# Performance work log

Measured on AMD Instinct MI355X. Metric: run time of the kernel, lower is better.

The kernel has to match this reference:

```python
import jax, jax.numpy as jnp
import numpy as np
from jax import lax

K = 3
PAD = 1


def setup_inputs() -> dict:
    key = jax.random.key(0)
    k1, k2, k3 = jax.random.split(key, 3)
    B, Cin, Cout, H, W = 4, 64, 64, 128, 128
    x = jax.random.normal(k1, (B, Cin, H, W), dtype=jnp.float32)
    # offset-predicting conv params (2*K*K output channels); small init keeps offsets modest
    offset_w = jax.random.normal(k2, (2 * K * K, Cin, K, K), dtype=jnp.float32) * 0.05
    offset_b = jnp.zeros((2 * K * K,), dtype=jnp.float32)
    # deformable conv weight/bias (module uses randn weight, zero bias)
    weight = jax.random.normal(k3, (Cout, Cin, K, K), dtype=jnp.float32) * 0.05
    bias = jnp.zeros((Cout,), dtype=jnp.float32)
    return {"x": x, "offset_w": offset_w, "offset_b": offset_b, "weight": weight, "bias": bias}


def _conv2d(x, w, b):
    y = lax.conv_general_dilated(x, w, window_strides=(1, 1),
                                 padding=((PAD, PAD), (PAD, PAD)),
                                 dimension_numbers=("NCHW", "OIHW", "NCHW"))
    return y + b[None, :, None, None]


def _bilinear_gather(x, py, px):
    # x: [B,C,H,W]; py,px: [B,KK,HO,WO] sample coords -> [B,C,KK,HO,WO], zeros outside
    B, C, H, W = x.shape
    y0 = jnp.floor(py)
    x0 = jnp.floor(px)
    ly = py - y0
    lx = px - x0
    y0i = y0.astype(jnp.int32)
    x0i = x0.astype(jnp.int32)
    xf = x.reshape(B, C, H * W)

    def corner(yi, xi, w):
        mask = ((yi >= 0) & (yi < H) & (xi >= 0) & (xi < W)).astype(x.dtype)
        lin = jnp.clip(yi, 0, H - 1) * W + jnp.clip(xi, 0, W - 1)  # [B,KK,HO,WO]
        g = jax.vmap(lambda xb, ib: xb[:, ib])(xf, lin)            # [B,C,KK,HO,WO]
        return g * (w * mask)[:, None]

    return (corner(y0i, x0i, (1 - ly) * (1 - lx))
            + corner(y0i, x0i + 1, (1 - ly) * lx)
            + corner(y0i + 1, x0i, ly * (1 - lx))
            + corner(y0i + 1, x0i + 1, ly * lx))


def reference(x, offset_w, offset_b, weight, bias):
    B, Cin, H, W = x.shape
    Cout = weight.shape[0]
    KK = K * K
    offset = _conv2d(x, offset_w, offset_b)            # [B, 2*KK, H, W]
    off = offset.reshape(B, KK, 2, H, W)               # torchvision layout: (dy, dx) per tap
    dy, dx = off[:, :, 0], off[:, :, 1]                # [B,KK,H,W]
    ki = (jnp.arange(KK) // K).astype(x.dtype)
    kj = (jnp.arange(KK) % K).astype(x.dtype)
    hs = jnp.arange(H, dtype=x.dtype)
    ws = jnp.arange(W, dtype=x.dtype)
    base_y = ki[:, None, None] + hs[None, :, None] - PAD   # [KK,H,1]
    base_x = kj[:, None, None] + ws[None, None, :] - PAD   # [KK,1,W]
    py = dy + base_y[None]                             # [B,KK,H,W]
    px = dx + base_x[None]
    sampled = _bilinear_gather(x, py, px)              # [B,Cin,KK,H,W]
    out = jnp.einsum("bckhw,ock->bohw", sampled, weight.reshape(Cout, Cin, KK))
    return out + bias[None, :, None, None]
```

## Files before the change

kernel.cpp:

```cpp
#include <hip/hip_runtime.h>

typedef _Float16 f16x8 __attribute__((ext_vector_type(8)));
typedef float f32x4 __attribute__((ext_vector_type(4)));

__device__ __forceinline__ f16x8 splat8(float v) {
  _Float16 h = (_Float16)v;
  return f16x8{h, h, h, h, h, h, h, h};
}

__device__ __forceinline__ int swzh(int i) { return i ^ (((i >> 6) & 7) << 3); }

__global__ __launch_bounds__(256) void k_xtprep(const float* __restrict__ x,
                                                const float* __restrict__ wt,
                                                const float* __restrict__ ow,
                                                _Float16* __restrict__ xt,
                                                _Float16* __restrict__ wb,
                                                _Float16* __restrict__ owb) {
  __shared__ float tile[64 * 65];
  int blk = blockIdx.x;
  int t = threadIdx.x;
  if (blk < 1024) {
    int b = blk >> 8;
    int y = (blk >> 1) & 127;
    int w0 = (blk & 1) * 64;
    const float* xp = x + ((size_t)(b * 64) * 128 + y) * 128 + w0;
#pragma unroll
    for (int it = 0; it < 4; ++it) {
      int idx = it * 256 + t;
      int c = idx >> 4, q = idx & 15;
      float4 v = *(const float4*)(xp + (size_t)c * 16384 + q * 4);
      float* tp = &tile[c * 65 + q * 4];
      tp[0] = v.x; tp[1] = v.y; tp[2] = v.z; tp[3] = v.w;
    }
    __syncthreads();
#pragma unroll
    for (int it = 0; it < 2; ++it) {
      int idx = it * 256 + t;
      int w = idx >> 3, c8 = idx & 7;
      f16x8 o;
#pragma unroll
      for (int j = 0; j < 8; ++j) o[j] = (_Float16)tile[(c8 * 8 + j) * 65 + w];
      *(f16x8*)&xt[(((size_t)b * 128 + y) * 128 + w0 + w) * 64 + c8 * 8] = o;
    }
  } else {
    int i = (blk - 1024) * 256 + t;
    if (i < 36864) {
      int k = i >> 12, rem = i & 4095, o = rem >> 6, c = rem & 63;
      wb[i] = (_Float16)wt[(o * 64 + c) * 9 + k];
    } else if (i < 36864 + 18432) {
      int j = i - 36864;
      int k = j >> 11, rem = j & 2047, o = rem >> 6, c = rem & 63;
      float v = (o < 18) ? ow[(o * 64 + c) * 9 + k] : 0.0f;
      owb[j] = (_Float16)v;
    }
  }
}

__global__ __launch_bounds__(512, 2) void k_fused(
    const _Float16* __restrict__ xt, const _Float16* __restrict__ wb,
    const _Float16* __restrict__ owb, const float* __restrict__ ob,
    const float* __restrict__ bias, float* __restrict__ out) {
  __shared__ char lds[75776];
  _Float16* Wp3 = (_Float16*)lds;
  _Float16* S = (_Float16*)(lds + 49152);
  _Float16* Xs = (_Float16*)lds;
  _Float16* owbL = (_Float16*)(lds + 26112);
  float* offL = (float*)(lds + 65536);

  int t = threadIdx.x;
  int lb = (blockIdx.x & 7) * 64 + (blockIdx.x >> 3);
  int w0 = (lb & 3) * 32;
  int h0 = ((lb >> 2) & 31) * 4;
  int b = lb >> 7;

  int lane = t & 63, wid = t >> 6;
  int lr = lane & 15, quad = lane >> 4;
  const _Float16* xb = xt + (size_t)b * 128 * 128 * 64;

#pragma unroll
  for (int it = 0; it < 4; ++it) {
    int idx8 = it * 512 + t;
    if (idx8 < 1632) {
      int c8 = idx8 & 7;
      int jr = idx8 >> 3;
      int col = jr % 34;
      int xr = jr / 34;
      int gy = h0 - 1 + xr;
      int gx = w0 - 1 + col;
      f16x8 v = {};
      if (((unsigned)gy < 128u) & ((unsigned)gx < 128u))
        v = *(const f16x8*)(xb + ((size_t)gy * 128 + gx) * 64 + c8 * 8);
      *(f16x8*)&Xs[swzh(jr * 64 + c8 * 8)] = v;
    }
  }
#pragma unroll
  for (int it = 0; it < 2; ++it) {
    int idx8 = it * 512 + t;
    if (idx8 < 768) {
      int kb = idx8 >> 8, rem = idx8 & 255;
      int o = rem >> 3, c8 = rem & 7;
      *(f16x8*)&owbL[swzh(kb * 2048 + o * 64 + c8 * 8)] =
          ((const f16x8*)(owb + kb * 2048))[rem];
    }
  }

  {
    int oh = (wid >> 2) * 16;
    int ar = wid & 3;
    f32x4 accA[2];
    accA[0] = f32x4{0.f, 0.f, 0.f, 0.f};
    accA[1] = f32x4{0.f, 0.f, 0.f, 0.f};
#pragma unroll
    for (int bt = 0; bt < 3; ++bt) {
      __syncthreads();
#pragma unroll
      for (int kb = 0; kb < 3; ++kb) {
        int ai = (bt & 1) * 6144 + kb * 2048 + (oh + lr) * 64 + quad * 8;
        f16x8 afr0 = *(const f16x8*)&owbL[swzh(ai)];
        f16x8 afr1 = *(const f16x8*)&owbL[swzh(ai + 32)];
#pragma unroll
        for (int ni = 0; ni < 2; ++ni) {
          int j = ni * 16 + lr + kb;
          int bi = ((ar + bt) * 34 + j) * 64 + quad * 8;
          f16x8 b0 = *(const f16x8*)&Xs[swzh(bi)];
          f16x8 b1 = *(const f16x8*)&Xs[swzh(bi + 32)];
          accA[ni] = __builtin_amdgcn_mfma_f32_16x16x32_f16(afr0, b0, accA[ni], 0, 0, 0);
          accA[ni] = __builtin_amdgcn_mfma_f32_16x16x32_f16(afr1, b1, accA[ni], 0, 0, 0);
        }
      }
      if (bt < 2) {
#pragma unroll
        for (int it = 0; it < 2; ++it) {
          int idx8 = it * 512 + t;
          if (idx8 < 768) {
            int kb = idx8 >> 8, rem = idx8 & 255;
            int o = rem >> 3, c8 = rem & 7;
            *(f16x8*)&owbL[swzh(((bt + 1) & 1) * 6144 + kb * 2048 + o * 64 + c8 * 8)] =
                ((const f16x8*)(owb + ((bt + 1) * 3 + kb) * 2048))[rem];
          }
        }
      }
    }
    int qr = quad * 4;
#pragma unroll
    for (int ni = 0; ni < 2; ++ni) {
#pragma unroll
      for (int r = 0; r < 4; ++r) {
        int co = oh + qr + r;
        if (co < 18) {
          int px = ar * 32 + ni * 16 + lr;
          offL[px * 20 + co] = accA[ni][r] + ob[co];
        }
      }
    }
  }
  __syncthreads();

  int pixS = t >> 2, cg = t & 3;
  int rS = pixS >> 5;
  int wS = w0 + (pixS & 31);
  int woB = (wid >> 2) * 32, wpB = (wid & 3) * 32;

  f32x4 acc[2][2];
#pragma unroll
  for (int i = 0; i < 2; ++i)
#pragma unroll
    for (int j = 0; j < 2; ++j) acc[i][j] = f32x4{0.f, 0.f, 0.f, 0.f};

#pragma unroll
  for (int it = 0; it < 3; ++it) {
    int idx8 = it * 512 + t;
    int kb = idx8 >> 9, rem = idx8 & 511;
    int o = rem >> 3, c8 = rem & 7;
    *(f16x8*)&Wp3[swzh(kb * 4096 + o * 64 + c8 * 8)] =
        ((const f16x8*)(wb + kb * 4096))[rem];
  }

#pragma unroll
  for (int k = 0; k < 9; ++k) {
    if (k == 1 || k == 4) {
      int bt = k / 3 + 1;
#pragma unroll
      for (int it = 0; it < 3; ++it) {
        int idx8 = it * 512 + t;
        int kb = idx8 >> 9, rem = idx8 & 511;
        int o = rem >> 3, c8 = rem & 7;
        *(f16x8*)&Wp3[swzh((bt & 1) * 12288 + kb * 4096 + o * 64 + c8 * 8)] =
            ((const f16x8*)(wb + (bt * 3 + kb) * 4096))[rem];
      }
    }
    {
      int ki = k / 3, kj = k % 3;
      float dy = offL[pixS * 20 + 2 * k];
      float dx = offL[pixS * 20 + 2 * k + 1];
      float py = dy + (float)(h0 + rS + ki - 1);
      float pxf = dx + (float)(wS + kj - 1);
      float fy = floorf(py), fx = floorf(pxf);
      float ly = py - fy, lx = pxf - fx;
      int y0 = (int)fy, x0 = (int)fx;
      int y1 = y0 + 1, x1 = x0 + 1;
      bool vy0 = (unsigned)y0 < 128u, vy1 = (unsigned)y1 < 128u;
      bool vx0 = (unsigned)x0 < 128u, vx1 = (unsigned)x1 < 128u;
      float w00 = (vy0 && vx0) ? (1.f - ly) * (1.f - lx) : 0.f;
      float w01 = (vy0 && vx1) ? (1.f - ly) * lx : 0.f;
      float w10 = (vy1 && vx0) ? ly * (1.f - lx) : 0.f;
      float w11 = (vy1 && vx1) ? ly * lx : 0.f;
      int yc0 = min(max(y0, 0), 127), yc1 = min(max(y1, 0), 127);
      int xc0 = min(max(x0, 0), 127), xc1 = min(max(x1, 0), 127);
      const _Float16* p00 = xb + (yc0 * 128 + xc0) * 64 + cg * 16;
      int dxo = (xc1 - xc0) * 64, dyo = (yc1 - yc0) * 8192;
      f16x8 ga0 = *(const f16x8*)(p00);
      f16x8 ga1 = *(const f16x8*)(p00 + 8);
      f16x8 gb0 = *(const f16x8*)(p00 + dxo);
      f16x8 gb1 = *(const f16x8*)(p00 + dxo + 8);
      f16x8 gc0 = *(const f16x8*)(p00 + dyo);
      f16x8 gc1 = *(const f16x8*)(p00 + dyo + 8);
      f16x8 gd0 = *(const f16x8*)(p00 + dyo + dxo);
      f16x8 gd1 = *(const f16x8*)(p00 + dyo + dxo + 8);
      f16x8 W00 = splat8(w00), W01 = splat8(w01);
      f16x8 W10 = splat8(w10), W11 = splat8(w11);
      f16x8 s0 = W00 * ga0 + W01 * gb0 + W10 * gc0 + W11 * gd0;
      f16x8 s1 = W00 * ga1 + W01 * gb1 + W10 * gc1 + W11 * gd1;
      int si = pixS * 64 + cg * 16;
      *(f16x8*)&S[swzh(si)] = s0;
      *(f16x8*)&S[swzh(si + 8)] = s1;
    }
    __syncthreads();
    {
      int wo = ((k / 3) & 1) * 12288 + (k % 3) * 4096;
#pragma unroll
      for (int ks = 0; ks < 2; ++ks) {
        int c0 = ks * 32 + quad * 8;
        f16x8 bfr[2], afr[2];
#pragma unroll
        for (int ni = 0; ni < 2; ++ni)
          bfr[ni] = *(const f16x8*)&S[swzh((wpB + ni * 16 + lr) * 64 + c0)];
#pragma unroll
        for (int mi = 0; mi < 2; ++mi)
          afr[mi] = *(const f16x8*)&Wp3[swzh(wo + (woB + mi * 16 + lr) * 64 + c0)];
#pragma unroll
        for (int mi = 0; mi < 2; ++mi)
#pragma unroll
          for (int ni = 0; ni < 2; ++ni)
            acc[mi][ni] = __builtin_amdgcn_mfma_f32_16x16x32_f16(
                afr[mi], bfr[ni], acc[mi][ni], 0, 0, 0);
      }
    }
    if (k < 8) __syncthreads();
  }

  {
    int col = lane & 15;
    int qr = quad * 4;
#pragma unroll
    for (int mi = 0; mi < 2; ++mi) {
#pragma unroll
      for (int ni = 0; ni < 2; ++ni) {
#pragma unroll
        for (int r = 0; r < 4; ++r) {
          int o = woB + mi * 16 + qr + r;
          int px = wpB + ni * 16 + col;
          out[(((size_t)b * 64 + o) * 128 + h0 + (px >> 5)) * 128 + w0 + (px & 31)] =
              acc[mi][ni][r] + bias[o];
        }
      }
    }
  }
}

extern "C" void kernel_launch(void* const* d_in, const int* in_sizes, int n_in,
                              void* d_out, int out_size, void* d_ws,
                              size_t ws_size, hipStream_t stream) {
  const float* x = (const float*)d_in[0];
  const float* ow = (const float*)d_in[1];
  const float* ob = (const float*)d_in[2];
  const float* wt = (const float*)d_in[3];
  const float* bias = (const float*)d_in[4];
  float* out = (float*)d_out;

  char* ws = (char*)d_ws;
  _Float16* xt = (_Float16*)ws;
  _Float16* wb = (_Float16*)(ws + 8388608);
  _Float16* owb = (_Float16*)(ws + 8388608 + 73728);

  k_xtprep<<<1240, 256, 0, stream>>>(x, wt, ow, xt, wb, owb);
  k_fused<<<512, 512, 0, stream>>>(xt, wb, owb, ob, bias, out);
}
```

Measured before the change: 35.82 us.

## Warp-specialize deform conv: producer waves sample next tap while consumers run MFMA

Splits the 8 waves into 4 producer waves that stage one tap's weights and bilinear-sample the next tap into a double-buffered LDS tile, and 4 consumer waves that run MFMAs on the current tap covering all 64 output channels. The aim is to overlap gather latency with matrix math and to shrink LDS from three-tap weight staging to two single-tap buffers. In exchange, half the threads do sampling, so each producer handles twice the channels, and consumers carry a larger accumulator tile. The critical path may become whichever role is slower.

```diff
diff --git a/kernel.cpp b/kernel.cpp
--- a/kernel.cpp
+++ b/kernel.cpp
@@ -60,12 +60,12 @@
     const _Float16* __restrict__ xt, const _Float16* __restrict__ wb,
     const _Float16* __restrict__ owb, const float* __restrict__ ob,
     const float* __restrict__ bias, float* __restrict__ out) {
-  __shared__ char lds[75776];
-  _Float16* Wp3 = (_Float16*)lds;
-  _Float16* S = (_Float16*)(lds + 49152);
+  __shared__ char lds[60928];
+  _Float16* Wt2 = (_Float16*)lds;
+  _Float16* S2 = (_Float16*)(lds + 16384);
   _Float16* Xs = (_Float16*)lds;
   _Float16* owbL = (_Float16*)(lds + 26112);
-  float* offL = (float*)(lds + 65536);
+  float* offL = (float*)(lds + 50688);
 
   int t = threadIdx.x;
   int lb = (blockIdx.x & 7) * 64 + (blockIdx.x >> 3);
@@ -156,109 +156,120 @@
   }
   __syncthreads();
 
-  int pixS = t >> 2, cg = t & 3;
-  int rS = pixS >> 5;
-  int wS = w0 + (pixS & 31);
-  int woB = (wid >> 2) * 32, wpB = (wid & 3) * 32;
-
-  f32x4 acc[2][2];
-#pragma unroll
-  for (int i = 0; i < 2; ++i)
+  int st = t & 255;
+  int pxS = st & 127, chh = st >> 7;
+  int rS = pxS >> 5;
+  int wS = w0 + (pxS & 31);
+  int wpB = (wid & 3) * 32;
+
+  f32x4 acc[4][2];
+#pragma unroll
+  for (int i = 0; i < 4; ++i)
 #pragma unroll
     for (int j = 0; j < 2; ++j) acc[i][j] = f32x4{0.f, 0.f, 0.f, 0.f};
 
-#pragma unroll
-  for (int it = 0; it < 3; ++it) {
-    int idx8 = it * 512 + t;
-    int kb = idx8 >> 9, rem = idx8 & 511;
-    int o = rem >> 3, c8 = rem & 7;
-    *(f16x8*)&Wp3[swzh(kb * 4096 + o * 64 + c8 * 8)] =
-        ((const f16x8*)(wb + kb * 4096))[rem];
-  }
+#define STAGE_W_TAP(KK)                                                       \
+  {                                                                           \
+    const f16x8* wsrc = (const f16x8*)(wb + (KK) * 4096);                     \
+    _Pragma("unroll") for (int it = 0; it < 2; ++it) {                        \
+      int idx8 = it * 256 + st;                                               \
+      int o = idx8 >> 3, c8 = idx8 & 7;                                       \
+      *(f16x8*)&Wt2[((KK) & 1) * 4096 + swzh(o * 64 + c8 * 8)] = wsrc[idx8];  \
+    }                                                                         \
+  }
+
+#define SAMPLE_TAP(KK)                                                        \
+  {                                                                           \
+    int ki = (KK) / 3, kj = (KK) % 3;                                         \
+    float dy = offL[pxS * 20 + 2 * (KK)];                                     \
+    float dx = offL[pxS * 20 + 2 * (KK) + 1];                                 \
+    float py = dy + (float)(h0 + rS + ki - 1);                                \
+    float pxf = dx + (float)(wS + kj - 1);                                    \
+    float fy = floorf(py), fx = floorf(pxf);                                  \
+    float ly = py - fy, lx = pxf - fx;                                        \
+    int y0 = (int)fy, x0 = (int)fx;                                           \
+    int y1 = y0 + 1, x1 = x0 + 1;                                             \
+    bool vy0 = (unsigned)y0 < 128u, vy1 = (unsigned)y1 < 128u;                \
+    bool vx0 = (unsigned)x0 < 128u, vx1 = (unsigned)x1 < 128u;                \
+    float w00 = (vy0 && vx0) ? (1.f - ly) * (1.f - lx) : 0.f;                 \
+    float w01 = (vy0 && vx1) ? (1.f - ly) * lx : 0.f;                         \
+    float w10 = (vy1 && vx0) ? ly * (1.f - lx) : 0.f;                         \
+    float w11 = (vy1 && vx1) ? ly * lx : 0.f;                                 \
+    int yc0 = min(max(y0, 0), 127), yc1 = min(max(y1, 0), 127);               \
+    int xc0 = min(max(x0, 0), 127), xc1 = min(max(x1, 0), 127);               \
+    const _Float16* p00 = xb + (yc0 * 128 + xc0) * 64 + chh * 32;             \
+    int dxo = (xc1 - xc0) * 64, dyo = (yc1 - yc0) * 8192;                     \
+    f16x8 g0[4], g1[4], g2[4], g3[4];                                         \
+    _Pragma("unroll") for (int j = 0; j < 4; ++j) {                           \
+      g0[j] = *(const f16x8*)(p00 + j * 8);                                   \
+      g1[j] = *(const f16x8*)(p00 + dxo + j * 8);                             \
+      g2[j] = *(const f16x8*)(p00 + dyo + j * 8);                             \
+      g3[j] = *(const f16x8*)(p00 + dyo + dxo + j * 8);                       \
+    }                                                                         \
+    f16x8 W00 = splat8(w00), W01 = splat8(w01);                               \
+    f16x8 W10 = splat8(w10), W11 = splat8(w11);                               \
+    _Float16* Sd = (_Float16*)&S2[((KK) & 1) * 8192];                         \
+    _Pragma("unroll") for (int j = 0; j < 4; ++j) {                           \
+      f16x8 s = W00 * g0[j] + W01 * g1[j] + W10 * g2[j] + W11 * g3[j];        \
+      *(f16x8*)&Sd[swzh(pxS * 64 + chh * 32 + j * 8)] = s;                    \
+    }                                                                         \
+  }
+
+  if (wid >= 4) {
+    STAGE_W_TAP(0)
+    SAMPLE_TAP(0)
+  }
+  __syncthreads();
 
 #pragma unroll
   for (int k = 0; k < 9; ++k) {
-    if (k == 1 || k == 4) {
-      int bt = k / 3 + 1;
-#pragma unroll
-      for (int it = 0; it < 3; ++it) {
-        int idx8 = it * 512 + t;
-        int kb = idx8 >> 9, rem = idx8 & 511;
-        int o = rem >> 3, c8 = rem & 7;
-        *(f16x8*)&Wp3[swzh((bt & 1) * 12288 + kb * 4096 + o * 64 + c8 * 8)] =
-            ((const f16x8*)(wb + (bt * 3 + kb) * 4096))[rem];
-      }
-    }
-    {
-      int ki = k / 3, kj = k % 3;
-      float dy = offL[pixS * 20 + 2 * k];
-      float dx = offL[pixS * 20 + 2 * k + 1];
-      float py = dy + (float)(h0 + rS + ki - 1);
-      float pxf = dx + (float)(wS + kj - 1);
-      float fy = floorf(py), fx = floorf(pxf);
-      float ly = py - fy, lx = pxf - fx;
-      int y0 = (int)fy, x0 = (int)fx;
-      int y1 = y0 + 1, x1 = x0 + 1;
-      bool vy0 = (unsigned)y0 < 128u, vy1 = (unsigned)y1 < 128u;
-      bool vx0 = (unsigned)x0 < 128u, vx1 = (unsigned)x1 < 128u;
-      float w00 = (vy0 && vx0) ? (1.f - ly) * (1.f - lx) : 0.f;
-      float w01 = (vy0 && vx1) ? (1.f - ly) * lx : 0.f;
-      float w10 = (vy1 && vx0) ? ly * (1.f - lx) : 0.f;
-      float w11 = (vy1 && vx1) ? ly * lx : 0.f;
-      int yc0 = min(max(y0, 0), 127), yc1 = min(max(y1, 0), 127);
-      int xc0 = min(max(x0, 0), 127), xc1 = min(max(x1, 0), 127);
-      const _Float16* p00 = xb + (yc0 * 128 + xc0) * 64 + cg * 16;
-      int dxo = (xc1 - xc0) * 64, dyo = (yc1 - yc0) * 8192;
-      f16x8 ga0 = *(const f16x8*)(p00);
-      f16x8 ga1 = *(const f16x8*)(p00 + 8);
-      f16x8 gb0 = *(const f16x8*)(p00 + dxo);
-      f16x8 gb1 = *(const f16x8*)(p00 + dxo + 8);
-      f16x8 gc0 = *(const f16x8*)(p00 + dyo);
-      f16x8 gc1 = *(const f16x8*)(p00 + dyo + 8);
-      f16x8 gd0 = *(const f16x8*)(p00 + dyo + dxo);
-      f16x8 gd1 = *(const f16x8*)(p00 + dyo + dxo + 8);
-      f16x8 W00 = splat8(w00), W01 = splat8(w01);
-      f16x8 W10 = splat8(w10), W11 = splat8(w11);
-      f16x8 s0 = W00 * ga0 + W01 * gb0 + W10 * gc0 + W11 * gd0;
-      f16x8 s1 = W00 * ga1 + W01 * gb1 + W10 * gc1 + W11 * gd1;
-      int si = pixS * 64 + cg * 16;
-      *(f16x8*)&S[swzh(si)] = s0;
-      *(f16x8*)&S[swzh(si + 8)] = s1;
-    }
-    __syncthreads();
-    {
-      int wo = ((k / 3) & 1) * 12288 + (k % 3) * 4096;
+    if (wid < 4) {
+      const _Float16* Wc = &Wt2[(k & 1) * 4096];
+      const _Float16* Sc = &S2[(k & 1) * 8192];
 #pragma unroll
       for (int ks = 0; ks < 2; ++ks) {
         int c0 = ks * 32 + quad * 8;
-        f16x8 bfr[2], afr[2];
+        f16x8 bfr[2], afr[4];
 #pragma unroll
         for (int ni = 0; ni < 2; ++ni)
-          bfr[ni] = *(const f16x8*)&S[swzh((wpB + ni * 16 + lr) * 64 + c0)];
-#pragma unroll
-        for (int mi = 0; mi < 2; ++mi)
-          afr[mi] = *(const f16x8*)&Wp3[swzh(wo + (woB + mi * 16 + lr) * 64 + c0)];
-#pragma unroll
-        for (int mi = 0; mi < 2; ++mi)
+          bfr[ni] = *(const f16x8*)&Sc[swzh((wpB + ni * 16 + lr) * 64 + c0)];
+#pragma unroll
+        for (int mi = 0; mi < 4; ++mi)
+          afr[mi] = *(const f16x8*)&Wc[swzh((mi * 16 + lr) * 64 + c0)];
+#pragma unroll
+        for (int mi = 0; mi < 4; ++mi)
 #pragma unroll
           for (int ni = 0; ni < 2; ++ni)
             acc[mi][ni] = __builtin_amdgcn_mfma_f32_16x16x32_f16(
                 afr[mi], bfr[ni], acc[mi][ni], 0, 0, 0);
       }
-    }
-    if (k < 8) __syncthreads();
-  }
-
-  {
+    } else if (k < 8) {
+      switch (k + 1) {
+        case 1: STAGE_W_TAP(1) SAMPLE_TAP(1) break;
+        case 2: STAGE_W_TAP(2) SAMPLE_TAP(2) break;
+        case 3: STAGE_W_TAP(3) SAMPLE_TAP(3) break;
+        case 4: STAGE_W_TAP(4) SAMPLE_TAP(4) break;
+        case 5: STAGE_W_TAP(5) SAMPLE_TAP(5) break;
+        case 6: STAGE_W_TAP(6) SAMPLE_TAP(6) break;
+        case 7: STAGE_W_TAP(7) SAMPLE_TAP(7) break;
+        case 8: STAGE_W_TAP(8) SAMPLE_TAP(8) break;
+      }
+    }
+    __syncthreads();
+  }
+#undef SAMPLE_TAP
+#undef STAGE_W_TAP
+
+  if (wid < 4) {
     int col = lane & 15;
     int qr = quad * 4;
 #pragma unroll
-    for (int mi = 0; mi < 2; ++mi) {
+    for (int mi = 0; mi < 4; ++mi) {
 #pragma unroll
       for (int ni = 0; ni < 2; ++ni) {
 #pragma unroll
         for (int r = 0; r < 4; ++r) {
-          int o = woB + mi * 16 + qr + r;
+          int o = mi * 16 + qr + r;
           int px = wpB + ni * 16 + col;
           out[(((size_t)b * 64 + o) * 128 + h0 + (px >> 5)) * 128 + w0 + (px & 31)] =
               acc[mi][ni][r] + bias[o];
```

After: 57.21 us. 59.7% more time.
